# Kernel tuning notes

Measured on AMD Instinct MI355X. Metric: run time of the kernel, lower is better.

Reference implementation:

```python
import jax, jax.numpy as jnp
import numpy as np

DMODEL = 2048
HEADS = 16
DHEAD = DMODEL // HEADS  # 128


def setup_inputs() -> dict:
    key = jax.random.key(0)
    ks = jax.random.split(key, 9)
    s = 0.02
    x = jax.random.normal(ks[0], (4, 2048, DMODEL), dtype=jnp.float32)
    Wq = jax.random.normal(ks[1], (DMODEL, DMODEL), dtype=jnp.float32) * s
    bq = jax.random.normal(ks[2], (DMODEL,), dtype=jnp.float32) * s
    Wk = jax.random.normal(ks[3], (DMODEL, DMODEL), dtype=jnp.float32) * s
    bk = jax.random.normal(ks[4], (DMODEL,), dtype=jnp.float32) * s
    Wv = jax.random.normal(ks[5], (DMODEL, DMODEL), dtype=jnp.float32) * s
    bv = jax.random.normal(ks[6], (DMODEL,), dtype=jnp.float32) * s
    Wo = jax.random.normal(ks[7], (DMODEL, DMODEL), dtype=jnp.float32) * s
    bo = jax.random.normal(ks[8], (DMODEL,), dtype=jnp.float32) * s
    return {"x": x, "Wq": Wq, "bq": bq, "Wk": Wk, "bk": bk, "Wv": Wv, "bv": bv, "Wo": Wo, "bo": bo}


def reference(x, Wq, bq, Wk, bk, Wv, bv, Wo, bo):
    b, l, _ = x.shape
    # projections: [b, l, dmodel] -> [b, l, heads, dhead]
    q = (x @ Wq + bq).reshape(b, l, HEADS, DHEAD)
    k = (x @ Wk + bk).reshape(b, l, HEADS, DHEAD)
    v = (x @ Wv + bv).reshape(b, l, HEADS, DHEAD)
    # NOTE: source applies 1/sqrt(dhead) twice -> total scale 1/dhead (faithful)
    a = jnp.einsum('blhd,bLhd->bhlL', q, k) * (1.0 / DHEAD)
    a = jax.nn.softmax(a, axis=-1)
    prefinal = jnp.einsum('bhlL,bLhd->blhd', a, v)
    out = prefinal.reshape(b, l, HEADS * DHEAD) @ Wo + bo
    return out
```

## Files before the change

### kernel.cpp

```cpp
#include <hip/hip_runtime.h>

#define DMODEL 2048
#define SEQ    2048
#define BATCH  4
#define HEADS  16
#define DHEAD  128

typedef __attribute__((ext_vector_type(8))) short short8;
typedef __attribute__((ext_vector_type(4))) float f32x4;
typedef __attribute__((ext_vector_type(16))) float f32x16;

__device__ __forceinline__ unsigned short f2bf(float f) {
  union { float f; unsigned u; } v; v.f = f;
  unsigned r = v.u + 0x7FFFu + ((v.u >> 16) & 1u);
  return (unsigned short)(r >> 16);
}

__global__ __launch_bounds__(256) void cvt_f32_bf16(const float* __restrict__ in,
                                                    unsigned short* __restrict__ out,
                                                    int n4) {
  int i = blockIdx.x * 256 + threadIdx.x;
  if (i >= n4) return;
  float4 v = ((const float4*)in)[i];
  ushort4 o;
  o.x = f2bf(v.x); o.y = f2bf(v.y); o.z = f2bf(v.z); o.w = f2bf(v.w);
  ((ushort4*)out)[i] = o;
}

__global__ __launch_bounds__(256) void transpose_cvt4(const float* __restrict__ w0,
                                                      const float* __restrict__ w1,
                                                      const float* __restrict__ w2,
                                                      const float* __restrict__ w3,
                                                      unsigned short* __restrict__ o0,
                                                      unsigned short* __restrict__ o1,
                                                      unsigned short* __restrict__ o2,
                                                      unsigned short* __restrict__ o3) {
  __shared__ float tile[32][33];
  const int z = blockIdx.z;
  const float* in = (z == 0) ? w0 : (z == 1) ? w1 : (z == 2) ? w2 : w3;
  unsigned short* out = (z == 0) ? o0 : (z == 1) ? o1 : (z == 2) ? o2 : o3;
  const int tx = threadIdx.x, ty = threadIdx.y;
  const int x = blockIdx.x * 32 + tx;
  const int y0 = blockIdx.y * 32;
#pragma unroll
  for (int j = 0; j < 32; j += 8)
    tile[ty + j][tx] = in[(size_t)(y0 + ty + j) * DMODEL + x];
  __syncthreads();
  const int xo = blockIdx.y * 32 + tx;
  const int yo0 = blockIdx.x * 32;
#pragma unroll
  for (int j = 0; j < 32; j += 8)
    out[(size_t)(yo0 + ty + j) * DMODEL + xo] = f2bf(tile[tx][ty + j]);
}

__global__ __launch_bounds__(256) void transpose_v(const unsigned short* __restrict__ in,
                                                   unsigned short* __restrict__ out) {
  __shared__ unsigned short t[32][33];
  const int tx = threadIdx.x, ty = threadIdx.y;
  const int bid = blockIdx.x;
  const int lb = bid & 63;
  const int db = (bid >> 6) & 3;
  const int h  = (bid >> 8) & 15;
  const int b  = bid >> 12;
#pragma unroll
  for (int j = 0; j < 32; j += 8)
    t[ty + j][tx] = in[(size_t)(b * SEQ + lb * 32 + ty + j) * DMODEL + h * DHEAD + db * 32 + tx];
  __syncthreads();
  const size_t ob = ((size_t)(b * HEADS + h) * DHEAD + db * 32) * SEQ + lb * 32;
#pragma unroll
  for (int j = 0; j < 32; j += 8)
    out[ob + (size_t)(ty + j) * SEQ + tx] = t[tx][ty + j];
}

template <typename OUT_T, int NTN>
__global__ __launch_bounds__(512, 2) void gemm2(const unsigned short* __restrict__ A,
                                                const unsigned short* __restrict__ Bt,
                                                const float* __restrict__ b0,
                                                const float* __restrict__ b1,
                                                const float* __restrict__ b2,
                                                OUT_T* __restrict__ C) {
  __shared__ unsigned short As[2][256 * 64];
  __shared__ unsigned short Bs[2][256 * 64];

  const int tid = threadIdx.x;
  const int l = tid & 63, w = tid >> 6;
  const int wr = w >> 2, wc = w & 3;

  const int bid = blockIdx.x;
  int tm, tn;
  if constexpr (NTN == 24) {
    const int xcd = bid & 7;
    const int idx = bid >> 3;
    const int r = xcd >> 1, c = xcd & 1;
    const int mt = idx >> 4;
    const int i = idx & 15;
    const int mrow = mt & 1, mcol = mt >> 1;
    tm = r * 8 + mrow * 4 + (i & 3);
    tn = c * 12 + mcol * 4 + (i >> 2);
  } else {
    const int q8 = (32 * NTN) >> 3;
    const int swz = (bid & 7) * q8 + (bid >> 3);
    tn = swz % NTN;
    tm = swz / NTN;
  }

  const int srow = w * 8 + (l >> 3);
  const int schunk = (l & 7) ^ (l >> 3);
  const unsigned short* Ag = A + (size_t)(tm * 256 + srow) * DMODEL + schunk * 8;
  const unsigned short* Bg = Bt + (size_t)(tn * 256 + srow) * DMODEL + schunk * 8;

#define GLL(src, dst) __builtin_amdgcn_global_load_lds( \
    (const __attribute__((address_space(1))) void*)(src), \
    (__attribute__((address_space(3))) void*)(dst), 16, 0, 0)

#define STAGE_A(bf, kt) do { \
    GLL(Ag + (size_t)0 * 64 * DMODEL + (kt) * 64,   &As[bf][0 * 4096 + w * 512]); \
    GLL(Ag + (size_t)1 * 64 * DMODEL + (kt) * 64,   &As[bf][1 * 4096 + w * 512]); \
    GLL(Ag + (size_t)2 * 64 * DMODEL + (kt) * 64,   &As[bf][2 * 4096 + w * 512]); \
    GLL(Ag + (size_t)3 * 64 * DMODEL + (kt) * 64,   &As[bf][3 * 4096 + w * 512]); \
  } while (0)
#define STAGE_B(bf, kt) do { \
    GLL(Bg + (size_t)0 * 64 * DMODEL + (kt) * 64,   &Bs[bf][0 * 4096 + w * 512]); \
    GLL(Bg + (size_t)1 * 64 * DMODEL + (kt) * 64,   &Bs[bf][1 * 4096 + w * 512]); \
    GLL(Bg + (size_t)2 * 64 * DMODEL + (kt) * 64,   &Bs[bf][2 * 4096 + w * 512]); \
    GLL(Bg + (size_t)3 * 64 * DMODEL + (kt) * 64,   &Bs[bf][3 * 4096 + w * 512]); \
  } while (0)

  f32x4 acc[8][4] = {};

  STAGE_A(0, 0);
  STAGE_B(0, 0);
  int buf = 0;
  for (int t = 0; t < 32; ++t) {
    __builtin_amdgcn_s_barrier();
    __builtin_amdgcn_sched_barrier(0);
    if (t < 31) {
      STAGE_A(buf ^ 1, t + 1);
      __builtin_amdgcn_sched_barrier(0);
      asm volatile("s_waitcnt vmcnt(4)" ::: "memory");
    } else {
      asm volatile("s_waitcnt vmcnt(0)" ::: "memory");
    }
    __builtin_amdgcn_sched_barrier(0);
    __builtin_amdgcn_s_barrier();
    __builtin_amdgcn_sched_barrier(0);

    {
      const unsigned short* Asb = &As[buf][0];
      const unsigned short* Bsb = &Bs[buf][0];
      short8 bfr[4][2];
#pragma unroll
      for (int n = 0; n < 4; ++n) {
        const int row = wc * 64 + n * 16 + (l & 15);
#pragma unroll
        for (int ks = 0; ks < 2; ++ks)
          bfr[n][ks] = *(const short8*)&Bsb[row * 64 + (((ks * 4 + (l >> 4)) ^ (row & 7)) * 8)];
      }

#define COMPUTE_HALF(mb) do { \
        __builtin_amdgcn_s_setprio(1); \
        _Pragma("unroll") \
        for (int mi = 0; mi < 4; ++mi) { \
          const int m = (mb) + mi; \
          const int row = wr * 128 + m * 16 + (l & 15); \
          short8 af0 = *(const short8*)&Asb[row * 64 + (((0 + (l >> 4)) ^ (row & 7)) * 8)]; \
          short8 af1 = *(const short8*)&Asb[row * 64 + (((4 + (l >> 4)) ^ (row & 7)) * 8)]; \
          _Pragma("unroll") \
          for (int n = 0; n < 4; ++n) { \
            acc[m][n] = __builtin_amdgcn_mfma_f32_16x16x32_bf16(af0, bfr[n][0], acc[m][n], 0, 0, 0); \
            acc[m][n] = __builtin_amdgcn_mfma_f32_16x16x32_bf16(af1, bfr[n][1], acc[m][n], 0, 0, 0); \
          } \
        } \
        __builtin_amdgcn_s_setprio(0); \
      } while (0)

      if (w & 1) {
        COMPUTE_HALF(4);
        if (t < 31) STAGE_B(buf ^ 1, t + 1);
        COMPUTE_HALF(0);
      } else {
        COMPUTE_HALF(0);
        if (t < 31) STAGE_B(buf ^ 1, t + 1);
        COMPUTE_HALF(4);
      }
#undef COMPUTE_HALF
    }
    buf ^= 1;
  }
#undef STAGE_A
#undef STAGE_B
#undef GLL

  const int bsel = tn >> 3;
  const float* bp = (bsel == 0) ? b0 : ((bsel == 1) ? b1 : b2);
  OUT_T* Cb = C + (size_t)bsel * ((size_t)8192 * DMODEL);
  const int row0 = tm * 256 + wr * 128 + ((l >> 4) * 4);
  const int lc0 = (tn & 7) * 256 + wc * 64 + (l & 15);
#pragma unroll
  for (int n = 0; n < 4; ++n) {
    float bv = bp[lc0 + n * 16];
#pragma unroll
    for (int m = 0; m < 8; ++m) {
#pragma unroll
      for (int r = 0; r < 4; ++r) {
        float v = acc[m][n][r] + bv;
        size_t idx = (size_t)(row0 + m * 16 + r) * DMODEL + (lc0 + n * 16);
        if constexpr (sizeof(OUT_T) == 2) ((unsigned short*)Cb)[idx] = f2bf(v);
        else                              ((float*)Cb)[idx] = v;
      }
    }
  }
}

__global__ __launch_bounds__(256) void attn(const unsigned short* __restrict__ Q,
                                            const unsigned short* __restrict__ K,
                                            const unsigned short* __restrict__ V,
                                            unsigned short* __restrict__ O) {
  __shared__ unsigned short Ks[32 * 136];
  __shared__ unsigned short Vt[128 * 40];
  __shared__ unsigned short Ps[4][16 * 40];

  const int tid = threadIdx.x;
  const int l = tid & 63, w = tid >> 6;
  const int bh = blockIdx.x >> 5, qb = blockIdx.x & 31;
  const int b = bh >> 4, h = bh & 15;
  const size_t base = ((size_t)b * SEQ) * DMODEL + (size_t)h * DHEAD;

  const unsigned short* Qp = Q + base + (size_t)(qb * 64 + w * 16) * DMODEL;
  short8 qf[4];
#pragma unroll
  for (int dc = 0; dc < 4; ++dc)
    qf[dc] = *(const short8*)(Qp + (size_t)(l & 15) * DMODEL + dc * 32 + (l >> 4) * 8);

  f32x4 acc[8] = {};
  float sum[4] = {0.f, 0.f, 0.f, 0.f};

  const int skv = tid >> 3;
  const int sc = (tid & 7) * 16;
  const unsigned short* Kg = K + base + (size_t)skv * DMODEL + sc;
  const unsigned short* Vg = V + base + (size_t)skv * DMODEL + sc;

  const float cexp = 1.4426950408889634f / 128.0f;

  for (int kv0 = 0; kv0 < SEQ; kv0 += 32) {
    __syncthreads();
    short8 ka = *(const short8*)(Kg + (size_t)kv0 * DMODEL);
    short8 kb = *(const short8*)(Kg + (size_t)kv0 * DMODEL + 8);
    *(short8*)&Ks[skv * 136 + sc] = ka;
    *(short8*)&Ks[skv * 136 + sc + 8] = kb;
    short8 va = *(const short8*)(Vg + (size_t)kv0 * DMODEL);
    short8 vb = *(const short8*)(Vg + (size_t)kv0 * DMODEL + 8);
#pragma unroll
    for (int j = 0; j < 8; ++j) {
      Vt[(sc + j) * 40 + skv]     = (unsigned short)va[j];
      Vt[(sc + 8 + j) * 40 + skv] = (unsigned short)vb[j];
    }
    __syncthreads();

    f32x4 s[2];
#pragma unroll
    for (int nh = 0; nh < 2; ++nh) {
      f32x4 t = {};
#pragma unroll
      for (int dc = 0; dc < 4; ++dc) {
        short8 kf = *(const short8*)&Ks[(nh * 16 + (l & 15)) * 136 + dc * 32 + (l >> 4) * 8];
        t = __builtin_amdgcn_mfma_f32_16x16x32_bf16(qf[dc], kf, t, 0, 0, 0);
      }
      s[nh] = t;
    }

#pragma unroll
    for (int nh = 0; nh < 2; ++nh) {
#pragma unroll
      for (int r = 0; r < 4; ++r) {
        float p = exp2f(s[nh][r] * cexp);
        sum[r] += p;
        Ps[w][((l >> 4) * 4 + r) * 40 + (l & 15) + nh * 16] = f2bf(p);
      }
    }

    short8 pf = *(const short8*)&Ps[w][(l & 15) * 40 + (l >> 4) * 8];
#pragma unroll
    for (int db = 0; db < 8; ++db) {
      short8 vf = *(const short8*)&Vt[(db * 16 + (l & 15)) * 40 + (l >> 4) * 8];
      acc[db] = __builtin_amdgcn_mfma_f32_16x16x32_bf16(pf, vf, acc[db], 0, 0, 0);
    }
  }

  float inv[4];
#pragma unroll
  for (int r = 0; r < 4; ++r) {
    float s = sum[r];
    s += __shfl_xor(s, 1);
    s += __shfl_xor(s, 2);
    s += __shfl_xor(s, 4);
    s += __shfl_xor(s, 8);
    inv[r] = 1.0f / s;
  }
  unsigned short* Op = O + base + (size_t)(qb * 64 + w * 16) * DMODEL;
#pragma unroll
  for (int db = 0; db < 8; ++db)
#pragma unroll
    for (int r = 0; r < 4; ++r)
      Op[(size_t)((l >> 4) * 4 + r) * DMODEL + db * 16 + (l & 15)] = f2bf(acc[db][r] * inv[r]);
}

__global__ __launch_bounds__(256, 2) void attn6(const unsigned short* __restrict__ Q,
                                                const unsigned short* __restrict__ K,
                                                const unsigned short* __restrict__ VT,
                                                unsigned short* __restrict__ O) {
  __shared__ unsigned short Ks[2][64 * 128];
  __shared__ unsigned short Vs[2][128 * 64];

  const int tid = threadIdx.x;
  const int l = tid & 63, w = tid >> 6;
  const int x32 = l & 31, h = l >> 5;

  const int bid = blockIdx.x;
  const int swz = (bid & 7) * 64 + (bid >> 3);
  const int bh = swz >> 3, qb = swz & 7;
  const int b = bh >> 4, hh = bh & 15;
  const size_t base = ((size_t)b * SEQ) * DMODEL + (size_t)hh * DHEAD;
  const unsigned short* VTb = VT + (size_t)bh * DHEAD * SEQ;

  const unsigned short* Qp = Q + base + (size_t)(qb * 256 + w * 64) * DMODEL;
  short8 qfA[8], qfB[8];
#pragma unroll
  for (int dc = 0; dc < 8; ++dc) {
    qfA[dc] = *(const short8*)(Qp + (size_t)x32 * DMODEL + dc * 16 + h * 8);
    qfB[dc] = *(const short8*)(Qp + (size_t)(x32 + 32) * DMODEL + dc * 16 + h * 8);
  }

  const unsigned short* Kg0 = K + base + (size_t)(w * 16 + (l >> 4)) * DMODEL + (((l & 15) ^ (l >> 4)) * 8);
  const unsigned short* Kg1 = K + base + (size_t)(w * 16 + (l >> 4)) * DMODEL + (((l & 15) ^ ((l >> 4) + 4)) * 8);
  const unsigned short* Vg0 = VTb + (size_t)(w * 32 + (l >> 3)) * SEQ + (((l & 7) ^ (l >> 3)) * 8);

  unsigned short* KsD = &Ks[0][0];
  unsigned short* VsD = &Vs[0][0];

#define GLL(src, dst) __builtin_amdgcn_global_load_lds( \
    (const __attribute__((address_space(1))) void*)(src), \
    (__attribute__((address_space(3))) void*)(dst), 16, 0, 0)

#define STAGE(bf, kv0) do { \
    GLL(Kg0 + (size_t)(kv0) * DMODEL,        KsD + (bf) * 8192 + w * 2048 + 0 * 512); \
    GLL(Kg1 + (size_t)((kv0) + 4) * DMODEL,  KsD + (bf) * 8192 + w * 2048 + 1 * 512); \
    GLL(Kg0 + (size_t)((kv0) + 8) * DMODEL,  KsD + (bf) * 8192 + w * 2048 + 2 * 512); \
    GLL(Kg1 + (size_t)((kv0) + 12) * DMODEL, KsD + (bf) * 8192 + w * 2048 + 3 * 512); \
    GLL(Vg0 + (size_t)0 * SEQ + (kv0),       VsD + (bf) * 8192 + w * 2048 + 0 * 512); \
    GLL(Vg0 + (size_t)8 * SEQ + (kv0),       VsD + (bf) * 8192 + w * 2048 + 1 * 512); \
    GLL(Vg0 + (size_t)16 * SEQ + (kv0),      VsD + (bf) * 8192 + w * 2048 + 2 * 512); \
    GLL(Vg0 + (size_t)24 * SEQ + (kv0),      VsD + (bf) * 8192 + w * 2048 + 3 * 512); \
  } while (0)

  f32x16 acc0[4] = {}, acc1[4] = {};
  float sum0 = 0.f, sum1 = 0.f;
  const float cexp = 1.4426950408889634f / 128.0f;

#define COMPUTE_SUB(bf, s) do { \
    const unsigned short* Kb_ = &Ks[bf][(s) * 32 * 128]; \
    const unsigned short* Vb_ = &Vs[bf][0]; \
    f32x16 sa0 = {}, sa1 = {}; \
    __builtin_amdgcn_s_setprio(1); \
    _Pragma("unroll") \
    for (int dc = 0; dc < 8; ++dc) { \
      short8 kf = *(const short8*)&Kb_[x32 * 128 + (((dc * 2 + h) ^ (x32 & 7)) * 8)]; \
      sa0 = __builtin_amdgcn_mfma_f32_32x32x16_bf16(kf, qfA[dc], sa0, 0, 0, 0); \
      sa1 = __builtin_amdgcn_mfma_f32_32x32x16_bf16(kf, qfB[dc], sa1, 0, 0, 0); \
    } \
    __builtin_amdgcn_s_setprio(0); \
    union { unsigned u[4]; short8 s8; } pf0A, pf1A, pf0B, pf1B; \
    { \
      float p[16]; \
      _Pragma("unroll") \
      for (int r = 0; r < 16; ++r) { p[r] = __builtin_amdgcn_exp2f(sa0[r] * cexp); sum0 += p[r]; } \
      unsigned pk0[4], pk1[4]; \
      _Pragma("unroll") \
      for (int blk = 0; blk < 4; ++blk) { \
        asm("v_cvt_pk_bf16_f32 %0, %1, %2" : "=v"(pk0[blk]) : "v"(p[blk * 4 + 0]), "v"(p[blk * 4 + 1])); \
        asm("v_cvt_pk_bf16_f32 %0, %1, %2" : "=v"(pk1[blk]) : "v"(p[blk * 4 + 2]), "v"(p[blk * 4 + 3])); \
      } \
      unsigned a0 = pk0[0], a1 = pk0[1], b0 = pk1[0], b1 = pk1[1]; \
      asm("v_permlane32_swap_b32 %0, %1" : "+v"(a0), "+v"(a1)); \
      asm("v_permlane32_swap_b32 %0, %1" : "+v"(b0), "+v"(b1)); \
      pf0A.u[0] = a0; pf0A.u[1] = b0; pf0A.u[2] = a1; pf0A.u[3] = b1; \
      unsigned c0 = pk0[2], c1 = pk0[3], d0 = pk1[2], d1 = pk1[3]; \
      asm("v_permlane32_swap_b32 %0, %1" : "+v"(c0), "+v"(c1)); \
      asm("v_permlane32_swap_b32 %0, %1" : "+v"(d0), "+v"(d1)); \
      pf1A.u[0] = c0; pf1A.u[1] = d0; pf1A.u[2] = c1; pf1A.u[3] = d1; \
    } \
    { \
      float p[16]; \
      _Pragma("unroll") \
      for (int r = 0; r < 16; ++r) { p[r] = __builtin_amdgcn_exp2f(sa1[r] * cexp); sum1 += p[r]; } \
      unsigned pk0[4], pk1[4]; \
      _Pragma("unroll") \
      for (int blk = 0; blk < 4; ++blk) { \
        asm("v_cvt_pk_bf16_f32 %0, %1, %2" : "=v"(pk0[blk]) : "v"(p[blk * 4 + 0]), "v"(p[blk * 4 + 1])); \
        asm("v_cvt_pk_bf16_f32 %0, %1, %2" : "=v"(pk1[blk]) : "v"(p[blk * 4 + 2]), "v"(p[blk * 4 + 3])); \
      } \
      unsigned a0 = pk0[0], a1 = pk0[1], b0 = pk1[0], b1 = pk1[1]; \
      asm("v_permlane32_swap_b32 %0, %1" : "+v"(a0), "+v"(a1)); \
      asm("v_permlane32_swap_b32 %0, %1" : "+v"(b0), "+v"(b1)); \
      pf0B.u[0] = a0; pf0B.u[1] = b0; pf0B.u[2] = a1; pf0B.u[3] = b1; \
      unsigned c0 = pk0[2], c1 = pk0[3], d0 = pk1[2], d1 = pk1[3]; \
      asm("v_permlane32_swap_b32 %0, %1" : "+v"(c0), "+v"(c1)); \
      asm("v_permlane32_swap_b32 %0, %1" : "+v"(d0), "+v"(d1)); \
      pf1B.u[0] = c0; pf1B.u[1] = d0; pf1B.u[2] = c1; pf1B.u[3] = d1; \
    } \
    __builtin_amdgcn_s_setprio(1); \
    _Pragma("unroll") \
    for (int db = 0; db < 4; ++db) { \
      const int row = db * 32 + x32; \
      short8 vf0 = *(const short8*)&Vb_[row * 64 + ((((s) * 4 + 0 + h) ^ (row & 7)) * 8)]; \
      short8 vf1 = *(const short8*)&Vb_[row * 64 + ((((s) * 4 + 2 + h) ^ (row & 7)) * 8)]; \
      acc0[db] = __builtin_amdgcn_mfma_f32_32x32x16_bf16(pf0A.s8, vf0, acc0[db], 0, 0, 0); \
      acc1[db] = __builtin_amdgcn_mfma_f32_32x32x16_bf16(pf0B.s8, vf0, acc1[db], 0, 0, 0); \
      acc0[db] = __builtin_amdgcn_mfma_f32_32x32x16_bf16(pf1A.s8, vf1, acc0[db], 0, 0, 0); \
      acc1[db] = __builtin_amdgcn_mfma_f32_32x32x16_bf16(pf1B.s8, vf1, acc1[db], 0, 0, 0); \
    } \
    __builtin_amdgcn_s_setprio(0); \
  } while (0)

  STAGE(0, 0);
  int buf = 0;
  for (int t = 0; t < 32; ++t) {
    __builtin_amdgcn_s_barrier();
    __builtin_amdgcn_sched_barrier(0);
    if (t < 31) {
      STAGE(buf ^ 1, (t + 1) * 64);
      __builtin_amdgcn_sched_barrier(0);
      asm volatile("s_waitcnt vmcnt(8)" ::: "memory");
    } else {
      asm volatile("s_waitcnt vmcnt(0)" ::: "memory");
    }
    __builtin_amdgcn_sched_barrier(0);
    __builtin_amdgcn_s_barrier();
    __builtin_amdgcn_sched_barrier(0);
    COMPUTE_SUB(buf, 0);
    COMPUTE_SUB(buf, 1);
    buf ^= 1;
  }
#undef COMPUTE_SUB
#undef STAGE
#undef GLL

  sum0 += __shfl_xor(sum0, 32);
  sum1 += __shfl_xor(sum1, 32);
  float inv0 = 1.0f / sum0;
  float inv1 = 1.0f / sum1;
  float invq0[16], invq1[16];
#pragma unroll
  for (int r = 0; r < 16; ++r) {
    const int crow = (r & 3) + 8 * (r >> 2) + 4 * h;
    invq0[r] = __shfl(inv0, crow);
    invq1[r] = __shfl(inv1, crow);
  }

  unsigned short* Op = O + base + (size_t)(qb * 256 + w * 64) * DMODEL;
#pragma unroll
  for (int db = 0; db < 4; ++db)
#pragma unroll
    for (int r = 0; r < 16; ++r) {
      const int crow = (r & 3) + 8 * (r >> 2) + 4 * h;
      Op[(size_t)crow * DMODEL + db * 32 + x32] = f2bf(acc0[db][r] * invq0[r]);
      Op[(size_t)(crow + 32) * DMODEL + db * 32 + x32] = f2bf(acc1[db][r] * invq1[r]);
    }
}

extern "C" void kernel_launch(void* const* d_in, const int* in_sizes, int n_in,
                              void* d_out, int out_size, void* d_ws, size_t ws_size,
                              hipStream_t stream) {
  const float* x  = (const float*)d_in[0];
  const float* Wq = (const float*)d_in[1];
  const float* bq = (const float*)d_in[2];
  const float* Wk = (const float*)d_in[3];
  const float* bk = (const float*)d_in[4];
  const float* Wv = (const float*)d_in[5];
  const float* bv = (const float*)d_in[6];
  const float* Wo = (const float*)d_in[7];
  const float* bo = (const float*)d_in[8];

  char* ws = (char*)d_ws;
  unsigned short* xb  = (unsigned short*)ws;
  unsigned short* WqT = (unsigned short*)(ws + 33554432);
  unsigned short* WkT = (unsigned short*)(ws + 41943040);
  unsigned short* WvT = (unsigned short*)(ws + 50331648);
  unsigned short* WoT = (unsigned short*)(ws + 58720256);
  unsigned short* Qb  = (unsigned short*)(ws + 67108864);
  unsigned short* Kb  = (unsigned short*)(ws + 100663296);
  unsigned short* Vb  = (unsigned short*)(ws + 134217728);
  unsigned short* VTg = (unsigned short*)(ws + 167772160);
  unsigned short* Pf  = xb;

  const bool vt_ok = (ws_size >= (size_t)201326592);

  cvt_f32_bf16<<<16384, 256, 0, stream>>>(x, xb, (BATCH * SEQ * DMODEL) / 4);

  transpose_cvt4<<<dim3(64, 64, 4), dim3(32, 8), 0, stream>>>(Wq, Wk, Wv, Wo, WqT, WkT, WvT, WoT);

  gemm2<unsigned short, 24><<<768, 512, 0, stream>>>(xb, WqT, bq, bk, bv, Qb);

  if (vt_ok) {
    transpose_v<<<16384, dim3(32, 8), 0, stream>>>(Vb, VTg);
    attn6<<<512, 256, 0, stream>>>(Qb, Kb, VTg, Pf);
  } else {
    attn<<<2048, 256, 0, stream>>>(Qb, Kb, Vb, Pf);
  }

  gemm2<float, 8><<<256, 512, 0, stream>>>(Pf, WoT, bo, bo, bo, (float*)d_out);
}
```

Baseline: 537.0 us.

## Restructure GEMM main loop into four barrier-synchronized phases with finer-grained prefetch

Replaces the two-half compute loop of the projection and output GEMMs with a four-phase schedule. Each phase loads two A row-fragments, issues one A and one B global-to-LDS slice for the next k-tile, and runs 16 MFMAs between workgroup barriers. The last slice of tile t+2 is prefetched into the current buffer once it has been consumed. The aim is to interleave memory traffic evenly with MFMA work and keep waves in lockstep, at the cost of many more barriers per k-step and tighter reuse timing of LDS buffers.

```diff
diff --git a/kernel.cpp b/kernel.cpp
--- a/kernel.cpp
+++ b/kernel.cpp
@@ -73,12 +73,12 @@
 }
 
 template <typename OUT_T, int NTN>
-__global__ __launch_bounds__(512, 2) void gemm2(const unsigned short* __restrict__ A,
-                                                const unsigned short* __restrict__ Bt,
-                                                const float* __restrict__ b0,
-                                                const float* __restrict__ b1,
-                                                const float* __restrict__ b2,
-                                                OUT_T* __restrict__ C) {
+__global__ __launch_bounds__(512, 2) void gemm8p(const unsigned short* __restrict__ A,
+                                                 const unsigned short* __restrict__ Bt,
+                                                 const float* __restrict__ b0,
+                                                 const float* __restrict__ b1,
+                                                 const float* __restrict__ b2,
+                                                 OUT_T* __restrict__ C) {
   __shared__ unsigned short As[2][256 * 64];
   __shared__ unsigned short Bs[2][256 * 64];
 
@@ -112,83 +112,75 @@
 #define GLL(src, dst) __builtin_amdgcn_global_load_lds( \
     (const __attribute__((address_space(1))) void*)(src), \
     (__attribute__((address_space(3))) void*)(dst), 16, 0, 0)
-
-#define STAGE_A(bf, kt) do { \
-    GLL(Ag + (size_t)0 * 64 * DMODEL + (kt) * 64,   &As[bf][0 * 4096 + w * 512]); \
-    GLL(Ag + (size_t)1 * 64 * DMODEL + (kt) * 64,   &As[bf][1 * 4096 + w * 512]); \
-    GLL(Ag + (size_t)2 * 64 * DMODEL + (kt) * 64,   &As[bf][2 * 4096 + w * 512]); \
-    GLL(Ag + (size_t)3 * 64 * DMODEL + (kt) * 64,   &As[bf][3 * 4096 + w * 512]); \
-  } while (0)
-#define STAGE_B(bf, kt) do { \
-    GLL(Bg + (size_t)0 * 64 * DMODEL + (kt) * 64,   &Bs[bf][0 * 4096 + w * 512]); \
-    GLL(Bg + (size_t)1 * 64 * DMODEL + (kt) * 64,   &Bs[bf][1 * 4096 + w * 512]); \
-    GLL(Bg + (size_t)2 * 64 * DMODEL + (kt) * 64,   &Bs[bf][2 * 4096 + w * 512]); \
-    GLL(Bg + (size_t)3 * 64 * DMODEL + (kt) * 64,   &Bs[bf][3 * 4096 + w * 512]); \
-  } while (0)
+#define SGA(bf, i, kt) GLL(Ag + (size_t)(i) * 64 * DMODEL + (kt) * 64, &As[bf][(i) * 4096 + w * 512])
+#define SGB(bf, i, kt) GLL(Bg + (size_t)(i) * 64 * DMODEL + (kt) * 64, &Bs[bf][(i) * 4096 + w * 512])
 
   f32x4 acc[8][4] = {};
 
-  STAGE_A(0, 0);
-  STAGE_B(0, 0);
-  int buf = 0;
+  SGA(0, 0, 0); SGB(0, 0, 0);
+  SGA(0, 1, 0); SGB(0, 1, 0);
+  SGA(0, 2, 0); SGB(0, 2, 0);
+  SGA(0, 3, 0); SGB(0, 3, 0);
+  SGA(1, 0, 1); SGB(1, 0, 1);
+  __builtin_amdgcn_sched_barrier(0);
+  asm volatile("s_waitcnt vmcnt(2)" ::: "memory");
+  __builtin_amdgcn_s_barrier();
+  __builtin_amdgcn_sched_barrier(0);
+
   for (int t = 0; t < 32; ++t) {
-    __builtin_amdgcn_s_barrier();
-    __builtin_amdgcn_sched_barrier(0);
-    if (t < 31) {
-      STAGE_A(buf ^ 1, t + 1);
-      __builtin_amdgcn_sched_barrier(0);
-      asm volatile("s_waitcnt vmcnt(4)" ::: "memory");
-    } else {
-      asm volatile("s_waitcnt vmcnt(0)" ::: "memory");
-    }
-    __builtin_amdgcn_sched_barrier(0);
-    __builtin_amdgcn_s_barrier();
-    __builtin_amdgcn_sched_barrier(0);
-
-    {
-      const unsigned short* Asb = &As[buf][0];
-      const unsigned short* Bsb = &Bs[buf][0];
-      short8 bfr[4][2];
-#pragma unroll
-      for (int n = 0; n < 4; ++n) {
-        const int row = wc * 64 + n * 16 + (l & 15);
-#pragma unroll
-        for (int ks = 0; ks < 2; ++ks)
-          bfr[n][ks] = *(const short8*)&Bsb[row * 64 + (((ks * 4 + (l >> 4)) ^ (row & 7)) * 8)];
-      }
-
-#define COMPUTE_HALF(mb) do { \
-        __builtin_amdgcn_s_setprio(1); \
+    const int p = t & 1;
+    const unsigned short* Asb = &As[p][0];
+    const unsigned short* Bsb = &Bs[p][0];
+    short8 bfr[4][2];
+
+#define PHASE(Q) do { \
+      short8 af0_, af0b_, af1_, af1b_; \
+      { const int row0_ = wr * 128 + (2 * (Q)) * 16 + (l & 15); \
+        af0_  = *(const short8*)&Asb[row0_ * 64 + (((0 + (l >> 4)) ^ (row0_ & 7)) * 8)]; \
+        af0b_ = *(const short8*)&Asb[row0_ * 64 + (((4 + (l >> 4)) ^ (row0_ & 7)) * 8)]; \
+        const int row1_ = row0_ + 16; \
+        af1_  = *(const short8*)&Asb[row1_ * 64 + (((0 + (l >> 4)) ^ (row1_ & 7)) * 8)]; \
+        af1b_ = *(const short8*)&Asb[row1_ * 64 + (((4 + (l >> 4)) ^ (row1_ & 7)) * 8)]; } \
+      if ((Q) == 0) { \
         _Pragma("unroll") \
-        for (int mi = 0; mi < 4; ++mi) { \
-          const int m = (mb) + mi; \
-          const int row = wr * 128 + m * 16 + (l & 15); \
-          short8 af0 = *(const short8*)&Asb[row * 64 + (((0 + (l >> 4)) ^ (row & 7)) * 8)]; \
-          short8 af1 = *(const short8*)&Asb[row * 64 + (((4 + (l >> 4)) ^ (row & 7)) * 8)]; \
-          _Pragma("unroll") \
-          for (int n = 0; n < 4; ++n) { \
-            acc[m][n] = __builtin_amdgcn_mfma_f32_16x16x32_bf16(af0, bfr[n][0], acc[m][n], 0, 0, 0); \
-            acc[m][n] = __builtin_amdgcn_mfma_f32_16x16x32_bf16(af1, bfr[n][1], acc[m][n], 0, 0, 0); \
-          } \
+        for (int n = 0; n < 4; ++n) { \
+          const int row = wc * 64 + n * 16 + (l & 15); \
+          bfr[n][0] = *(const short8*)&Bsb[row * 64 + (((0 + (l >> 4)) ^ (row & 7)) * 8)]; \
+          bfr[n][1] = *(const short8*)&Bsb[row * 64 + (((4 + (l >> 4)) ^ (row & 7)) * 8)]; \
         } \
-        __builtin_amdgcn_s_setprio(0); \
-      } while (0)
-
-      if (w & 1) {
-        COMPUTE_HALF(4);
-        if (t < 31) STAGE_B(buf ^ 1, t + 1);
-        COMPUTE_HALF(0);
-      } else {
-        COMPUTE_HALF(0);
-        if (t < 31) STAGE_B(buf ^ 1, t + 1);
-        COMPUTE_HALF(4);
-      }
-#undef COMPUTE_HALF
-    }
-    buf ^= 1;
-  }
-#undef STAGE_A
-#undef STAGE_B
+      } \
+      if ((Q) < 3) { if (t < 31) { SGA(p ^ 1, (Q) + 1, t + 1); SGB(p ^ 1, (Q) + 1, t + 1); } } \
+      else         { if (t < 30) { SGA(p, 0, t + 2);           SGB(p, 0, t + 2); } } \
+      __builtin_amdgcn_sched_barrier(0); \
+      __builtin_amdgcn_s_barrier(); \
+      __builtin_amdgcn_sched_barrier(0); \
+      __builtin_amdgcn_s_setprio(1); \
+      _Pragma("unroll") \
+      for (int n = 0; n < 4; ++n) { \
+        acc[2 * (Q)][n]     = __builtin_amdgcn_mfma_f32_16x16x32_bf16(af0_,  bfr[n][0], acc[2 * (Q)][n], 0, 0, 0); \
+        acc[2 * (Q)][n]     = __builtin_amdgcn_mfma_f32_16x16x32_bf16(af0b_, bfr[n][1], acc[2 * (Q)][n], 0, 0, 0); \
+        acc[2 * (Q) + 1][n] = __builtin_amdgcn_mfma_f32_16x16x32_bf16(af1_,  bfr[n][0], acc[2 * (Q) + 1][n], 0, 0, 0); \
+        acc[2 * (Q) + 1][n] = __builtin_amdgcn_mfma_f32_16x16x32_bf16(af1b_, bfr[n][1], acc[2 * (Q) + 1][n], 0, 0, 0); \
+      } \
+      __builtin_amdgcn_s_setprio(0); \
+      if ((Q) == 3) { \
+        __builtin_amdgcn_sched_barrier(0); \
+        if (t < 30) asm volatile("s_waitcnt vmcnt(2)" ::: "memory"); \
+        else        asm volatile("s_waitcnt vmcnt(0)" ::: "memory"); \
+      } \
+      __builtin_amdgcn_sched_barrier(0); \
+      __builtin_amdgcn_s_barrier(); \
+      __builtin_amdgcn_sched_barrier(0); \
+    } while (0)
+
+    PHASE(0);
+    PHASE(1);
+    PHASE(2);
+    PHASE(3);
+#undef PHASE
+  }
+#undef SGA
+#undef SGB
 #undef GLL
 
   const int bsel = tn >> 3;
@@ -499,7 +491,7 @@
 
   transpose_cvt4<<<dim3(64, 64, 4), dim3(32, 8), 0, stream>>>(Wq, Wk, Wv, Wo, WqT, WkT, WvT, WoT);
 
-  gemm2<unsigned short, 24><<<768, 512, 0, stream>>>(xb, WqT, bq, bk, bv, Qb);
+  gemm8p<unsigned short, 24><<<768, 512, 0, stream>>>(xb, WqT, bq, bk, bv, Qb);
 
   if (vt_ok) {
     transpose_v<<<16384, dim3(32, 8), 0, stream>>>(Vb, VTg);
@@ -508,5 +500,5 @@
     attn<<<2048, 256, 0, stream>>>(Qb, Kb, Vb, Pf);
   }
 
-  gemm2<float, 8><<<256, 512, 0, stream>>>(Pf, WoT, bo, bo, bo, (float*)d_out);
-}
+  gemm8p<float, 8><<<256, 512, 0, stream>>>(Pf, WoT, bo, bo, bo, (float*)d_out);
+}
```

Result: faster. 499.3 us (-7.0%).
